# Kernel optimization log

Measured on AMD Instinct MI355X. Metric: run time of the kernel, lower is better.

Reference implementation:

```python
import jax, jax.numpy as jnp
import numpy as np

C = 64
D = C // 8  # query/key channels
B, H, W = 4, 64, 64


def setup_inputs() -> dict:
    key = jax.random.key(0)
    ks = jax.random.split(key, 8)
    x = jax.random.normal(ks[0], (B, C, H, W), dtype=jnp.float32)
    # 1x1 conv params (kernel squeezed to [out_ch, in_ch])
    sq = 1.0 / np.sqrt(C)
    Wq = jax.random.uniform(ks[1], (D, C), jnp.float32, -sq, sq)
    bq = jax.random.uniform(ks[2], (D,), jnp.float32, -sq, sq)
    Wk = jax.random.uniform(ks[3], (D, C), jnp.float32, -sq, sq)
    bk = jax.random.uniform(ks[4], (D,), jnp.float32, -sq, sq)
    Wv = jax.random.uniform(ks[5], (C, C), jnp.float32, -sq, sq)
    bv = jax.random.uniform(ks[6], (C,), jnp.float32, -sq, sq)
    # gamma is zero-initialized in the module; use a nonzero value so the
    # attention path actually contributes to the output.
    gamma = jax.random.normal(ks[7], (1,), dtype=jnp.float32)
    return {"x": x, "Wq": Wq, "bq": bq, "Wk": Wk, "bk": bk, "Wv": Wv, "bv": bv, "gamma": gamma}


def reference(x, Wq, bq, Wk, bk, Wv, bv, gamma):
    b, c, h, w = x.shape
    n = h * w
    xf = x.reshape(b, c, n)                                   # [B,C,N]
    q = jnp.einsum('dc,bcn->bdn', Wq, xf) + bq[None, :, None]  # [B,D,N]
    k = jnp.einsum('dc,bcn->bdn', Wk, xf) + bk[None, :, None]  # [B,D,N]
    v = jnp.einsum('ec,bcn->ben', Wv, xf) + bv[None, :, None]  # [B,C,N]
    energy = jnp.einsum('bdn,bdm->bnm', q, k)                  # [B,N,N] = Q^T K
    attn = jax.nn.softmax(energy, axis=-1)                     # softmax over keys m
    # out[b,c,n] = sum_m v[b,c,m] * attn[b,n,m]  (V @ attention^T in torch)
    out = jnp.einsum('bcm,bnm->bcn', v, attn).reshape(b, c, h, w)
    return gamma[0] * out + x
```

## Files before the change

kernel.cpp:

```cpp
#include <hip/hip_runtime.h>
#include <hip/hip_bf16.h>
#include <math.h>

#define BB 4
#define CC 64
#define DD 8
#define NN 4096
#define KS 4
#define KPS (NN / KS)
#define NT  (KPS / 128)
#define LOG2E 1.44269504088896340736f

typedef __attribute__((ext_vector_type(4))) short short4v;
typedef __attribute__((ext_vector_type(8))) unsigned short ushort8;
typedef __attribute__((ext_vector_type(16))) float f32x16;

#if defined(__HIP_DEVICE_COMPILE__)
  #if __has_builtin(__builtin_amdgcn_mfma_f32_32x32x8bf16_1k)
    #define MFMA32x8(A, B, C) __builtin_amdgcn_mfma_f32_32x32x8bf16_1k(A, B, C, 0, 0, 0)
  #elif __has_builtin(__builtin_amdgcn_mfma_f32_32x32x8_bf16)
    #define MFMA32x8(A, B, C) __builtin_amdgcn_mfma_f32_32x32x8_bf16(A, B, C, 0, 0, 0)
  #else
    #error "no 32x32x8 bf16 MFMA builtin in device pass"
  #endif
  #if __has_builtin(__builtin_amdgcn_exp2f)
    #define EXP2(x) __builtin_amdgcn_exp2f(x)
  #else
    #define EXP2(x) exp2f(x)
  #endif
#else
  static __device__ __host__ inline f32x16 MFMA32x8(short4v, short4v, f32x16 c) { return c; }
  #define EXP2(x) exp2f(x)
#endif

static __device__ inline short4v pack4(float a, float b, float c, float d) {
    union { short4v s; __hip_bfloat162 h[2]; } u;
    u.h[0] = __float22bfloat162_rn(make_float2(a, b));
    u.h[1] = __float22bfloat162_rn(make_float2(c, d));
    return u.s;
}

__global__ __launch_bounds__(256) void qkv_kernel(
    const float* __restrict__ x,  const float* __restrict__ Wq, const float* __restrict__ bq,
    const float* __restrict__ Wk, const float* __restrict__ bk,
    const float* __restrict__ Wv, const float* __restrict__ bv,
    unsigned short* __restrict__ qb, unsigned short* __restrict__ kb,
    unsigned short* __restrict__ vT)
{
    __shared__ unsigned short LQ[128 * 8];
    __shared__ unsigned short LK[128 * 8];

    int tid = threadIdx.x;
    int wave = tid >> 6, lane = tid & 63;
    int l32 = lane & 31, h2 = lane >> 5;

    int blk = blockIdx.x;
    int b = blk & (BB - 1);
    int r2 = blk >> 2;
    int rt = r2 % 3;
    int ng = r2 / 3;
    int n0 = ng * 128 + wave * 32;

    short4v af[8];
    #pragma unroll
    for (int s = 0; s < 8; ++s) {
        float4 w4;
        if (rt < 2) {
            w4 = *(const float4*)(Wv + (size_t)(rt * 32 + l32) * CC + s * 8 + 4 * h2);
        } else if (l32 < 8) {
            w4 = *(const float4*)(Wq + (size_t)l32 * CC + s * 8 + 4 * h2);
        } else if (l32 < 16) {
            w4 = *(const float4*)(Wk + (size_t)(l32 - 8) * CC + s * 8 + 4 * h2);
        } else {
            w4 = make_float4(0.f, 0.f, 0.f, 0.f);
        }
        af[s] = pack4(w4.x, w4.y, w4.z, w4.w);
    }

    const float* xb = x + (size_t)b * CC * NN + n0 + l32;
    short4v bf[8];
    #pragma unroll
    for (int s = 0; s < 8; ++s) {
        int c0 = s * 8 + 4 * h2;
        float x0 = xb[(size_t)(c0 + 0) * NN];
        float x1 = xb[(size_t)(c0 + 1) * NN];
        float x2 = xb[(size_t)(c0 + 2) * NN];
        float x3 = xb[(size_t)(c0 + 3) * NN];
        bf[s] = pack4(x0, x1, x2, x3);
    }

    f32x16 acc;
    #pragma unroll
    for (int r = 0; r < 16; ++r) acc[r] = 0.f;
    #pragma unroll
    for (int s = 0; s < 8; ++s)
        acc = MFMA32x8(af[s], bf[s], acc);

    if (rt < 2) {
        #pragma unroll
        for (int r = 0; r < 16; ++r) {
            int row = rt * 32 + (r & 3) + 8 * (r >> 2) + 4 * h2;
            float val = acc[r] + bv[row];
            __hip_bfloat16 hv = __float2bfloat16(val);
            vT[((size_t)b * CC + row) * NN + n0 + l32] = *(unsigned short*)&hv;
        }
    } else {
        short4v qp = pack4((acc[0] + bq[0 + 4 * h2]) * LOG2E,
                           (acc[1] + bq[1 + 4 * h2]) * LOG2E,
                           (acc[2] + bq[2 + 4 * h2]) * LOG2E,
                           (acc[3] + bq[3 + 4 * h2]) * LOG2E);
        short4v kp = pack4(acc[4] + bk[0 + 4 * h2],
                           acc[5] + bk[1 + 4 * h2],
                           acc[6] + bk[2 + 4 * h2],
                           acc[7] + bk[3 + 4 * h2]);
        int nl = wave * 32 + l32;
        *(short4v*)(LQ + (size_t)nl * 8 + 4 * h2) = qp;
        *(short4v*)(LK + (size_t)nl * 8 + 4 * h2) = kp;
        __syncthreads();
        if (tid < 128) {
            ushort8 row = *(const ushort8*)(LQ + (size_t)tid * 8);
            *(ushort8*)(qb + ((size_t)b * NN + ng * 128 + tid) * 8) = row;
        } else {
            int t = tid - 128;
            ushort8 row = *(const ushort8*)(LK + (size_t)t * 8);
            *(ushort8*)(kb + ((size_t)b * NN + ng * 128 + t) * 8) = row;
        }
    }
}

__global__ __launch_bounds__(256, 4) void flash_kernel(
    const unsigned short* __restrict__ qb, const unsigned short* __restrict__ kb,
    const unsigned short* __restrict__ vT, unsigned short* __restrict__ accb,
    float* __restrict__ sbuf)
{
    __shared__ unsigned short VS[2][64 * 132];
    int tid = threadIdx.x;
    int wave = tid >> 6, lane = tid & 63;
    int l32 = lane & 31, h2 = lane >> 5;

    int blk = blockIdx.x;
    int b = blk & (BB - 1);
    int rest = blk >> 2;
    int split = rest & (KS - 1);
    int qchunk = rest >> 2;
    int n0 = qchunk * 128 + wave * 32;

    short4v qf = *(const short4v*)(qb + ((size_t)b * NN + n0 + l32) * DD + h2 * 4);

    const unsigned short* kbb = kb + (size_t)b * NN * DD;
    const unsigned short* vbb = vT + (size_t)b * CC * NN;
    int m0 = split * KPS;

    int cch = tid >> 4, kg = tid & 15;
    int kgx = (kg ^ (cch & 3)) * 8;

    f32x16 o0, o1, zz;
    #pragma unroll
    for (int r = 0; r < 16; ++r) { o0[r] = 0.f; o1[r] = 0.f; zz[r] = 0.f; }
    float s0 = 0.f, s1 = 0.f, s2 = 0.f, s3 = 0.f;

    short4v kf[4];
    #pragma unroll
    for (int s = 0; s < 4; ++s)
        kf[s] = *(const short4v*)(kbb + (size_t)(m0 + s * 32 + l32) * DD + h2 * 4);
    ushort8 w0 = *(const ushort8*)(vbb + (size_t)(cch)      * NN + m0 + kg * 8);
    ushort8 w1 = *(const ushort8*)(vbb + (size_t)(16 + cch) * NN + m0 + kg * 8);
    ushort8 w2 = *(const ushort8*)(vbb + (size_t)(32 + cch) * NN + m0 + kg * 8);
    ushort8 w3 = *(const ushort8*)(vbb + (size_t)(48 + cch) * NN + m0 + kg * 8);
    *(ushort8*)(VS[0] + (size_t)(cch)      * 132 + kgx) = w0;
    *(ushort8*)(VS[0] + (size_t)(16 + cch) * 132 + kgx) = w1;
    *(ushort8*)(VS[0] + (size_t)(32 + cch) * 132 + kgx) = w2;
    *(ushort8*)(VS[0] + (size_t)(48 + cch) * 132 + kgx) = w3;

    int buf = 0;
    for (int tile = 0; tile < NT; ++tile) {
        __syncthreads();

        int mn = m0 + (tile + 1) * 128;
        short4v kn[4];
        #pragma unroll
        for (int s = 0; s < 4; ++s)
            kn[s] = *(const short4v*)(kbb + (size_t)(mn + s * 32 + l32) * DD + h2 * 4);
        w0 = *(const ushort8*)(vbb + (size_t)(cch)      * NN + mn + kg * 8);
        w1 = *(const ushort8*)(vbb + (size_t)(16 + cch) * NN + mn + kg * 8);
        w2 = *(const ushort8*)(vbb + (size_t)(32 + cch) * NN + mn + kg * 8);
        w3 = *(const ushort8*)(vbb + (size_t)(48 + cch) * NN + mn + kg * 8);

        const unsigned short* Vb = VS[buf];
        #pragma unroll
        for (int sub = 0; sub < 4; ++sub) {
            f32x16 st = MFMA32x8(kf[sub], qf, zz);
            float w[16];
            #pragma unroll
            for (int r = 0; r < 16; ++r) w[r] = EXP2(st[r]);
            s0 += (w[0] + w[1]) + (w[2] + w[3]);
            s1 += (w[4] + w[5]) + (w[6] + w[7]);
            s2 += (w[8] + w[9]) + (w[10] + w[11]);
            s3 += (w[12] + w[13]) + (w[14] + w[15]);

            union { short4v s; __hip_bfloat162 h[2]; } u[4];
            #pragma unroll
            for (int g = 0; g < 4; ++g) {
                u[g].h[0] = __float22bfloat162_rn(make_float2(w[4 * g],     w[4 * g + 1]));
                u[g].h[1] = __float22bfloat162_rn(make_float2(w[4 * g + 2], w[4 * g + 3]));
            }
            #pragma unroll
            for (int g = 0; g < 4; ++g) {
                int go = ((sub * 4 + g) ^ (l32 & 3)) * 8 + h2 * 4;
                short4v vf0 = *(const short4v*)(Vb + (size_t)(l32)      * 132 + go);
                short4v vf1 = *(const short4v*)(Vb + (size_t)(32 + l32) * 132 + go);
                o0 = MFMA32x8(u[g].s, vf0, o0);
                o1 = MFMA32x8(u[g].s, vf1, o1);
            }
        }

        if (tile != NT - 1) {
            unsigned short* Vn = VS[buf ^ 1];
            *(ushort8*)(Vn + (size_t)(cch)      * 132 + kgx) = w0;
            *(ushort8*)(Vn + (size_t)(16 + cch) * 132 + kgx) = w1;
            *(ushort8*)(Vn + (size_t)(32 + cch) * 132 + kgx) = w2;
            *(ushort8*)(Vn + (size_t)(48 + cch) * 132 + kgx) = w3;
            #pragma unroll
            for (int s = 0; s < 4; ++s) kf[s] = kn[s];
        }
        buf ^= 1;
    }

    __hip_bfloat16* ab = (__hip_bfloat16*)accb + (((size_t)(b * KS + split)) * NN + n0) * CC;
    #pragma unroll
    for (int r = 0; r < 16; ++r) {
        int qrow = (r & 3) + 8 * (r >> 2) + 4 * h2;
        ab[(size_t)qrow * CC + l32]      = __float2bfloat16(o0[r]);
        ab[(size_t)qrow * CC + 32 + l32] = __float2bfloat16(o1[r]);
    }
    float ssum = (s0 + s1) + (s2 + s3);
    ssum += __shfl_xor(ssum, 32);
    if (lane < 32)
        sbuf[(size_t)(b * KS + split) * NN + n0 + l32] = ssum;
}

__global__ __launch_bounds__(256) void norm_kernel(
    const unsigned short* __restrict__ accb, const float* __restrict__ sbuf,
    const float* __restrict__ x, const float* __restrict__ gamma,
    float* __restrict__ out)
{
    __shared__ float tile[32 * 65];
    __shared__ float stl[32];
    int blk = blockIdx.x;
    int b = blk >> 7;
    int n0 = (blk & 127) * 32;
    int tid = threadIdx.x;

    if (tid < 32) {
        float st = 0.f;
        #pragma unroll
        for (int sp = 0; sp < KS; ++sp)
            st += sbuf[(size_t)(b * KS + sp) * NN + n0 + tid];
        stl[tid] = 1.0f / st;
    }

    int nl = tid >> 3, cg = tid & 7;
    float a[8];
    #pragma unroll
    for (int e = 0; e < 8; ++e) a[e] = 0.f;
    #pragma unroll
    for (int sp = 0; sp < KS; ++sp) {
        ushort8 v = *(const ushort8*)(accb + (((size_t)(b * KS + sp) * NN) + n0 + nl) * CC + cg * 8);
        #pragma unroll
        for (int e = 0; e < 8; ++e)
            a[e] += __uint_as_float(((unsigned)v[e]) << 16);
    }
    #pragma unroll
    for (int e = 0; e < 8; ++e)
        tile[nl * 65 + cg * 8 + e] = a[e];
    __syncthreads();

    float g = gamma[0];
    #pragma unroll
    for (int p = 0; p < 8; ++p) {
        int idx = p * 256 + tid;
        int c = idx >> 5, n_l = idx & 31;
        size_t xi = ((size_t)b * CC + c) * NN + n0 + n_l;
        out[xi] = g * tile[n_l * 65 + c] * stl[n_l] + x[xi];
    }
}

extern "C" void kernel_launch(void* const* d_in, const int* in_sizes, int n_in,
                              void* d_out, int out_size, void* d_ws, size_t ws_size,
                              hipStream_t stream)
{
    const float* x     = (const float*)d_in[0];
    const float* Wq    = (const float*)d_in[1];
    const float* bq    = (const float*)d_in[2];
    const float* Wk    = (const float*)d_in[3];
    const float* bk    = (const float*)d_in[4];
    const float* Wv    = (const float*)d_in[5];
    const float* bv    = (const float*)d_in[6];
    const float* gamma = (const float*)d_in[7];
    float* out = (float*)d_out;

    float* ws = (float*)d_ws;
    size_t off = 0;
    unsigned short* qb = (unsigned short*)(ws + off); off += (size_t)BB * NN * DD / 2 + 64;
    unsigned short* kb = (unsigned short*)(ws + off); off += (size_t)BB * NN * DD / 2 + 64;
    unsigned short* vT = (unsigned short*)(ws + off); off += (size_t)BB * CC * NN / 2 + 64;
    unsigned short* accb = (unsigned short*)(ws + off); off += (size_t)BB * KS * NN * CC / 2 + 64;
    float* sbuf = ws + off; off += (size_t)BB * KS * NN;

    qkv_kernel<<<BB * 3 * 32, 256, 0, stream>>>(x, Wq, bq, Wk, bk, Wv, bv, qb, kb, vT);
    flash_kernel<<<BB * (NN / 128) * KS, 256, 0, stream>>>(qb, kb, vT, accb, sbuf);
    norm_kernel<<<BB * 128, 256, 0, stream>>>(accb, sbuf, x, gamma, out);
}
```

Baseline: 110.4 us.

## Double key splits, stage K/V in LDS per 256-key phase, pack partial outputs

Raises the key-split factor from 4 to 8, so each flash block covers 512 keys as two 256-key phases. Each phase's V and K tiles are staged through padded LDS buffers, with the second phase's global loads issued during the first phase's compute. The bf16 partial accumulators are written in the native MFMA register layout as packed pairs for coalesced stores, and the norm kernel is rewritten to read that layout. Doubling the grid improves occupancy and latency hiding, but doubles the partial-sum traffic the norm kernel must reduce.

```diff
diff --git a/kernel.cpp b/kernel.cpp
--- a/kernel.cpp
+++ b/kernel.cpp
@@ -6,12 +6,14 @@
 #define CC 64
 #define DD 8
 #define NN 4096
-#define KS 4
+#define KS 8
 #define KPS (NN / KS)
-#define NT  (KPS / 128)
+#define VSTR 260
+#define KSTR 12
 #define LOG2E 1.44269504088896340736f
 
 typedef __attribute__((ext_vector_type(4))) short short4v;
+typedef __attribute__((ext_vector_type(4))) unsigned short ushort4v;
 typedef __attribute__((ext_vector_type(8))) unsigned short ushort8;
 typedef __attribute__((ext_vector_type(16))) float f32x16;
 
@@ -38,6 +40,11 @@
     u.h[0] = __float22bfloat162_rn(make_float2(a, b));
     u.h[1] = __float22bfloat162_rn(make_float2(c, d));
     return u.s;
+}
+static __device__ inline unsigned packu(float lo, float hi) {
+    union { __hip_bfloat162 h; unsigned u; } t;
+    t.h = __float22bfloat162_rn(make_float2(lo, hi));
+    return t.u;
 }
 
 __global__ __launch_bounds__(256) void qkv_kernel(
@@ -130,10 +137,11 @@
 
 __global__ __launch_bounds__(256, 4) void flash_kernel(
     const unsigned short* __restrict__ qb, const unsigned short* __restrict__ kb,
-    const unsigned short* __restrict__ vT, unsigned short* __restrict__ accb,
+    const unsigned short* __restrict__ vT, unsigned* __restrict__ accb,
     float* __restrict__ sbuf)
 {
-    __shared__ unsigned short VS[2][64 * 132];
+    __shared__ unsigned short VS[64 * VSTR];
+    __shared__ unsigned short KL[256 * KSTR];
     int tid = threadIdx.x;
     int wave = tid >> 6, lane = tid & 63;
     int l32 = lane & 31, h2 = lane >> 5;
@@ -142,7 +150,7 @@
     int b = blk & (BB - 1);
     int rest = blk >> 2;
     int split = rest & (KS - 1);
-    int qchunk = rest >> 2;
+    int qchunk = rest >> 3;
     int n0 = qchunk * 128 + wave * 32;
 
     short4v qf = *(const short4v*)(qb + ((size_t)b * NN + n0 + l32) * DD + h2 * 4);
@@ -151,45 +159,44 @@
     const unsigned short* vbb = vT + (size_t)b * CC * NN;
     int m0 = split * KPS;
 
-    int cch = tid >> 4, kg = tid & 15;
-    int kgx = (kg ^ (cch & 3)) * 8;
+    int chb = wave * 16 + h2;
 
     f32x16 o0, o1, zz;
     #pragma unroll
     for (int r = 0; r < 16; ++r) { o0[r] = 0.f; o1[r] = 0.f; zz[r] = 0.f; }
     float s0 = 0.f, s1 = 0.f, s2 = 0.f, s3 = 0.f;
 
-    short4v kf[4];
-    #pragma unroll
-    for (int s = 0; s < 4; ++s)
-        kf[s] = *(const short4v*)(kbb + (size_t)(m0 + s * 32 + l32) * DD + h2 * 4);
-    ushort8 w0 = *(const ushort8*)(vbb + (size_t)(cch)      * NN + m0 + kg * 8);
-    ushort8 w1 = *(const ushort8*)(vbb + (size_t)(16 + cch) * NN + m0 + kg * 8);
-    ushort8 w2 = *(const ushort8*)(vbb + (size_t)(32 + cch) * NN + m0 + kg * 8);
-    ushort8 w3 = *(const ushort8*)(vbb + (size_t)(48 + cch) * NN + m0 + kg * 8);
-    *(ushort8*)(VS[0] + (size_t)(cch)      * 132 + kgx) = w0;
-    *(ushort8*)(VS[0] + (size_t)(16 + cch) * 132 + kgx) = w1;
-    *(ushort8*)(VS[0] + (size_t)(32 + cch) * 132 + kgx) = w2;
-    *(ushort8*)(VS[0] + (size_t)(48 + cch) * 132 + kgx) = w3;
-
-    int buf = 0;
-    for (int tile = 0; tile < NT; ++tile) {
-        __syncthreads();
-
-        int mn = m0 + (tile + 1) * 128;
-        short4v kn[4];
+    ushort8 vA[8];
+    #pragma unroll
+    for (int i = 0; i < 8; ++i)
+        vA[i] = *(const ushort8*)(vbb + (size_t)(chb + 2 * i) * NN + m0 + l32 * 8);
+    ushort8 kA = *(const ushort8*)(kbb + (size_t)(m0 + tid) * DD);
+    #pragma unroll
+    for (int i = 0; i < 8; ++i) {
+        unsigned short* p = VS + (size_t)(chb + 2 * i) * VSTR + l32 * 8;
+        *(ushort4v*)(p)     = *(ushort4v*)&vA[i];
+        *(ushort4v*)(p + 4) = *((ushort4v*)&vA[i] + 1);
+    }
+    {
+        unsigned short* p = KL + (size_t)tid * KSTR;
+        *(ushort4v*)(p)     = *(ushort4v*)&kA;
+        *(ushort4v*)(p + 4) = *((ushort4v*)&kA + 1);
+    }
+    __syncthreads();
+
+    int mB = m0 + 256;
+    ushort8 vB[8];
+    #pragma unroll
+    for (int i = 0; i < 8; ++i)
+        vB[i] = *(const ushort8*)(vbb + (size_t)(chb + 2 * i) * NN + mB + l32 * 8);
+    ushort8 kB = *(const ushort8*)(kbb + (size_t)(mB + tid) * DD);
+
+    #pragma unroll
+    for (int ph = 0; ph < 2; ++ph) {
         #pragma unroll
-        for (int s = 0; s < 4; ++s)
-            kn[s] = *(const short4v*)(kbb + (size_t)(mn + s * 32 + l32) * DD + h2 * 4);
-        w0 = *(const ushort8*)(vbb + (size_t)(cch)      * NN + mn + kg * 8);
-        w1 = *(const ushort8*)(vbb + (size_t)(16 + cch) * NN + mn + kg * 8);
-        w2 = *(const ushort8*)(vbb + (size_t)(32 + cch) * NN + mn + kg * 8);
-        w3 = *(const ushort8*)(vbb + (size_t)(48 + cch) * NN + mn + kg * 8);
-
-        const unsigned short* Vb = VS[buf];
-        #pragma unroll
-        for (int sub = 0; sub < 4; ++sub) {
-            f32x16 st = MFMA32x8(kf[sub], qf, zz);
+        for (int s = 0; s < 8; ++s) {
+            short4v kf = *(const short4v*)(KL + (size_t)(s * 32 + l32) * KSTR + h2 * 4);
+            f32x16 st = MFMA32x8(kf, qf, zz);
             float w[16];
             #pragma unroll
             for (int r = 0; r < 16; ++r) w[r] = EXP2(st[r]);
@@ -206,33 +213,33 @@
             }
             #pragma unroll
             for (int g = 0; g < 4; ++g) {
-                int go = ((sub * 4 + g) ^ (l32 & 3)) * 8 + h2 * 4;
-                short4v vf0 = *(const short4v*)(Vb + (size_t)(l32)      * 132 + go);
-                short4v vf1 = *(const short4v*)(Vb + (size_t)(32 + l32) * 132 + go);
+                int gg = s * 4 + g;
+                short4v vf0 = *(const short4v*)(VS + (size_t)(l32)      * VSTR + gg * 8 + h2 * 4);
+                short4v vf1 = *(const short4v*)(VS + (size_t)(32 + l32) * VSTR + gg * 8 + h2 * 4);
                 o0 = MFMA32x8(u[g].s, vf0, o0);
                 o1 = MFMA32x8(u[g].s, vf1, o1);
             }
         }
-
-        if (tile != NT - 1) {
-            unsigned short* Vn = VS[buf ^ 1];
-            *(ushort8*)(Vn + (size_t)(cch)      * 132 + kgx) = w0;
-            *(ushort8*)(Vn + (size_t)(16 + cch) * 132 + kgx) = w1;
-            *(ushort8*)(Vn + (size_t)(32 + cch) * 132 + kgx) = w2;
-            *(ushort8*)(Vn + (size_t)(48 + cch) * 132 + kgx) = w3;
+        if (ph == 0) {
+            __syncthreads();
             #pragma unroll
-            for (int s = 0; s < 4; ++s) kf[s] = kn[s];
-        }
-        buf ^= 1;
-    }
-
-    __hip_bfloat16* ab = (__hip_bfloat16*)accb + (((size_t)(b * KS + split)) * NN + n0) * CC;
-    #pragma unroll
-    for (int r = 0; r < 16; ++r) {
-        int qrow = (r & 3) + 8 * (r >> 2) + 4 * h2;
-        ab[(size_t)qrow * CC + l32]      = __float2bfloat16(o0[r]);
-        ab[(size_t)qrow * CC + 32 + l32] = __float2bfloat16(o1[r]);
-    }
+            for (int i = 0; i < 8; ++i) {
+                unsigned short* p = VS + (size_t)(chb + 2 * i) * VSTR + l32 * 8;
+                *(ushort4v*)(p)     = *(ushort4v*)&vB[i];
+                *(ushort4v*)(p + 4) = *((ushort4v*)&vB[i] + 1);
+            }
+            unsigned short* p = KL + (size_t)tid * KSTR;
+            *(ushort4v*)(p)     = *(ushort4v*)&kB;
+            *(ushort4v*)(p + 4) = *((ushort4v*)&kB + 1);
+            __syncthreads();
+        }
+    }
+
+    unsigned* au = accb + (((size_t)((b * KS + split) * 128 + qchunk * 4 + wave)) << 10);
+    #pragma unroll
+    for (int r = 0; r < 16; ++r)
+        au[r * 64 + lane] = packu(o0[r], o1[r]);
+
     float ssum = (s0 + s1) + (s2 + s3);
     ssum += __shfl_xor(ssum, 32);
     if (lane < 32)
@@ -240,7 +247,7 @@
 }
 
 __global__ __launch_bounds__(256) void norm_kernel(
-    const unsigned short* __restrict__ accb, const float* __restrict__ sbuf,
+    const unsigned* __restrict__ accb, const float* __restrict__ sbuf,
     const float* __restrict__ x, const float* __restrict__ gamma,
     float* __restrict__ out)
 {
@@ -248,7 +255,8 @@
     __shared__ float stl[32];
     int blk = blockIdx.x;
     int b = blk >> 7;
-    int n0 = (blk & 127) * 32;
+    int g = blk & 127;
+    int n0 = g * 32;
     int tid = threadIdx.x;
 
     if (tid < 32) {
@@ -259,29 +267,40 @@
         stl[tid] = 1.0f / st;
     }
 
-    int nl = tid >> 3, cg = tid & 7;
-    float a[8];
-    #pragma unroll
-    for (int e = 0; e < 8; ++e) a[e] = 0.f;
+    int r = tid >> 4;
+    int lane0 = (tid & 15) * 4;
+    int h2 = lane0 >> 5;
+    int qi = (r & 3) + 8 * (r >> 2) + 4 * h2;
+
+    float alo[4], ahi[4];
+    #pragma unroll
+    for (int e = 0; e < 4; ++e) { alo[e] = 0.f; ahi[e] = 0.f; }
     #pragma unroll
     for (int sp = 0; sp < KS; ++sp) {
-        ushort8 v = *(const ushort8*)(accb + (((size_t)(b * KS + sp) * NN) + n0 + nl) * CC + cg * 8);
+        const unsigned* base = accb + (((size_t)((b * KS + sp) * 128 + g)) << 10);
+        uint4 v = *(const uint4*)(base + tid * 4);
+        unsigned ws[4] = {v.x, v.y, v.z, v.w};
         #pragma unroll
-        for (int e = 0; e < 8; ++e)
-            a[e] += __uint_as_float(((unsigned)v[e]) << 16);
-    }
-    #pragma unroll
-    for (int e = 0; e < 8; ++e)
-        tile[nl * 65 + cg * 8 + e] = a[e];
+        for (int e = 0; e < 4; ++e) {
+            alo[e] += __uint_as_float(ws[e] << 16);
+            ahi[e] += __uint_as_float(ws[e] & 0xFFFF0000u);
+        }
+    }
+    #pragma unroll
+    for (int e = 0; e < 4; ++e) {
+        int cl = (lane0 + e) & 31;
+        tile[qi * 65 + cl]      = alo[e];
+        tile[qi * 65 + 32 + cl] = ahi[e];
+    }
     __syncthreads();
 
-    float g = gamma[0];
+    float gm = gamma[0];
     #pragma unroll
     for (int p = 0; p < 8; ++p) {
         int idx = p * 256 + tid;
         int c = idx >> 5, n_l = idx & 31;
         size_t xi = ((size_t)b * CC + c) * NN + n0 + n_l;
-        out[xi] = g * tile[n_l * 65 + c] * stl[n_l] + x[xi];
+        out[xi] = gm * tile[n_l * 65 + c] * stl[n_l] + x[xi];
     }
 }
 
@@ -304,7 +323,7 @@
     unsigned short* qb = (unsigned short*)(ws + off); off += (size_t)BB * NN * DD / 2 + 64;
     unsigned short* kb = (unsigned short*)(ws + off); off += (size_t)BB * NN * DD / 2 + 64;
     unsigned short* vT = (unsigned short*)(ws + off); off += (size_t)BB * CC * NN / 2 + 64;
-    unsigned short* accb = (unsigned short*)(ws + off); off += (size_t)BB * KS * NN * CC / 2 + 64;
+    unsigned* accb = (unsigned*)(ws + off); off += (size_t)BB * KS * NN * CC / 2;
     float* sbuf = ws + off; off += (size_t)BB * KS * NN;
 
     qkv_kernel<<<BB * 3 * 32, 256, 0, stream>>>(x, Wq, bq, Wk, bk, Wv, bv, qb, kb, vT);
```

New measurement: 113.4 us. +2.7%, slower.
